# Kernel optimization log

Measured on AMD Instinct MI355X. Metric: run time of the kernel, lower is better.

Reference implementation:

```python
import jax, jax.numpy as jnp
import numpy as np

TEMPERATURE = 0.5
EPS = 1e-8  # torch CosineSimilarity eps


def setup_inputs() -> dict:
    key = jax.random.key(0)
    # x holds 2*batch_size concatenated embeddings (two augmented views)
    x = jax.random.normal(key, (4096, 512), dtype=jnp.float32)
    return {"x": x}


def reference(x) -> jnp.ndarray:
    n2 = x.shape[0]          # 2N rows
    n = n2 // 2
    # cosine similarity: normalize rows (clamped norm as in torch), then GEMM
    norms = jnp.maximum(jnp.linalg.norm(x, axis=1, keepdims=True), EPS)
    xn = x / norms
    sim = jnp.einsum('id,jd->ij', xn, xn) / TEMPERATURE  # [2N, 2N]
    # positive logit for row i is sim[i, (i+N) mod 2N]
    idx = jnp.arange(n2)
    pos = sim[idx, (idx + n) % n2]
    # CE with label 0 over logits = [pos, negatives]; since the logit set for
    # row i is exactly {sim[i, j] : j != i}, CE_i = logsumexp_{j!=i} sim[i,j] - pos_i
    sim_masked = jnp.where(jnp.eye(n2, dtype=bool), -jnp.inf, sim)
    lse = jax.nn.logsumexp(sim_masked, axis=1)
    # criterion uses reduction='sum' then divides by bsz -> mean
    return jnp.mean(lse - pos)
```

## Files before the change

kernel.cpp:

```cpp
#include <hip/hip_runtime.h>
#include <hip/hip_bf16.h>
#include <math.h>

typedef __bf16 bf16_t;
typedef __bf16 bf16x8 __attribute__((ext_vector_type(8)));
typedef float f32x4 __attribute__((ext_vector_type(4)));

#define N2 4096
#define NHALF 2048
#define DIM 512
#define TEMP_INV 2.0f

__global__ __launch_bounds__(256) void k_prep(const float* __restrict__ x,
                                              bf16_t* __restrict__ xn,
                                              float* __restrict__ pos,
                                              float* __restrict__ diag,
                                              float* __restrict__ rowsum) {
    const int pair = blockIdx.x * 4 + (threadIdx.x >> 6);
    const int lane = threadIdx.x & 63;
    const int rowi = pair;
    const int rowp = pair + NHALF;

    const float4* xi = reinterpret_cast<const float4*>(x + (size_t)rowi * DIM);
    const float4* xp = reinterpret_cast<const float4*>(x + (size_t)rowp * DIM);
    float4 a0 = xi[lane * 2], a1 = xi[lane * 2 + 1];
    float4 b0 = xp[lane * 2], b1 = xp[lane * 2 + 1];

    float ssi = a0.x*a0.x + a0.y*a0.y + a0.z*a0.z + a0.w*a0.w
              + a1.x*a1.x + a1.y*a1.y + a1.z*a1.z + a1.w*a1.w;
    float ssp = b0.x*b0.x + b0.y*b0.y + b0.z*b0.z + b0.w*b0.w
              + b1.x*b1.x + b1.y*b1.y + b1.z*b1.z + b1.w*b1.w;
    float dot = a0.x*b0.x + a0.y*b0.y + a0.z*b0.z + a0.w*b0.w
              + a1.x*b1.x + a1.y*b1.y + a1.z*b1.z + a1.w*b1.w;
#pragma unroll
    for (int off = 32; off; off >>= 1) {
        ssi += __shfl_xor(ssi, off, 64);
        ssp += __shfl_xor(ssp, off, 64);
        dot += __shfl_xor(dot, off, 64);
    }
    const float ni = fmaxf(sqrtf(ssi), 1e-8f);
    const float np = fmaxf(sqrtf(ssp), 1e-8f);
    const float sci = 1.0f / ni, scp = 1.0f / np;

    float va[8] = {a0.x, a0.y, a0.z, a0.w, a1.x, a1.y, a1.z, a1.w};
    float vb[8] = {b0.x, b0.y, b0.z, b0.w, b1.x, b1.y, b1.z, b1.w};
    bf16x8 oi, op;
    float dii = 0.0f, dpp = 0.0f;
#pragma unroll
    for (int t = 0; t < 8; ++t) {
        oi[t] = (bf16_t)(va[t] * sci);
        op[t] = (bf16_t)(vb[t] * scp);
        float fi = (float)oi[t], fp_ = (float)op[t];
        dii += fi * fi;
        dpp += fp_ * fp_;
    }
    *reinterpret_cast<bf16x8*>(xn + (size_t)rowi * DIM + lane * 8) = oi;
    *reinterpret_cast<bf16x8*>(xn + (size_t)rowp * DIM + lane * 8) = op;
#pragma unroll
    for (int off = 32; off; off >>= 1) {
        dii += __shfl_xor(dii, off, 64);
        dpp += __shfl_xor(dpp, off, 64);
    }
    if (lane == 0) {
        const float pv = TEMP_INV * dot * sci * scp;
        pos[rowi] = pv;
        pos[rowp] = pv;
        diag[rowi] = TEMP_INV * dii;
        diag[rowp] = TEMP_INV * dpp;
    }
    if (threadIdx.x < 8) rowsum[blockIdx.x * 8 + threadIdx.x] = 0.0f;
}

__device__ __forceinline__ void load_lds16(const bf16_t* g, bf16_t* l) {
    __builtin_amdgcn_global_load_lds(
        (const __attribute__((address_space(1))) unsigned int*)g,
        (__attribute__((address_space(3))) unsigned int*)l,
        16, 0, 0);
}

__global__ __launch_bounds__(256) void k_simgemm(const bf16_t* __restrict__ xn,
                                                 float* __restrict__ rowsum) {
    __shared__ bf16_t As[2][128 * 64];
    __shared__ bf16_t Bs[2][128 * 64];
    __shared__ float  rpA[128];
    __shared__ float  rpB[128];

    const int t = blockIdx.x;
    int bn = (int)((sqrtf(8.0f * (float)t + 1.0f) - 1.0f) * 0.5f);
    while ((bn * (bn + 1)) / 2 > t) --bn;
    while (((bn + 1) * (bn + 2)) / 2 <= t) ++bn;
    const int bm = t - (bn * (bn + 1)) / 2;
    const bool diagb = (bm == bn);

    const int tid  = threadIdx.x;
    const int lane = tid & 63;
    const int wid  = tid >> 6;
    const int wr   = wid >> 1;
    const int wc   = wid & 1;
    const int q    = lane >> 4;
    const int l15  = lane & 15;

    if (tid < 128) { rpA[tid] = 0.0f; rpB[tid] = 0.0f; }

    const int sRow = tid >> 3;
    const int sCol = (tid & 7) * 8;
    const bf16_t* gA = xn + (size_t)(bm * 128 + sRow) * DIM + sCol;
    const bf16_t* gB = xn + (size_t)(bn * 128 + sRow) * DIM + sCol;

    f32x4 acc[4][4] = {};

#pragma unroll
    for (int c = 0; c < 4; ++c) {
        load_lds16(gA + (size_t)(c * 32) * DIM, &As[0][c * 2048 + tid * 8]);
        load_lds16(gB + (size_t)(c * 32) * DIM, &Bs[0][c * 2048 + tid * 8]);
    }
    __syncthreads();

    for (int kt = 0; kt < 8; ++kt) {
        const int cur = kt & 1;
        if (kt < 7) {
            const bf16_t* gA1 = gA + (size_t)(kt + 1) * 64;
            const bf16_t* gB1 = gB + (size_t)(kt + 1) * 64;
#pragma unroll
            for (int c = 0; c < 4; ++c) {
                load_lds16(gA1 + (size_t)(c * 32) * DIM,
                           &As[cur ^ 1][c * 2048 + tid * 8]);
                load_lds16(gB1 + (size_t)(c * 32) * DIM,
                           &Bs[cur ^ 1][c * 2048 + tid * 8]);
            }
        }
#pragma unroll
        for (int kk = 0; kk < 2; ++kk) {
            bf16x8 af[4], bv[4];
#pragma unroll
            for (int mt = 0; mt < 4; ++mt)
                af[mt] = *reinterpret_cast<const bf16x8*>(
                    &As[cur][(wr * 64 + mt * 16 + l15) * 64 + kk * 32 + q * 8]);
#pragma unroll
            for (int nt = 0; nt < 4; ++nt)
                bv[nt] = *reinterpret_cast<const bf16x8*>(
                    &Bs[cur][(wc * 64 + nt * 16 + l15) * 64 + kk * 32 + q * 8]);
#pragma unroll
            for (int mt = 0; mt < 4; ++mt)
#pragma unroll
                for (int nt = 0; nt < 4; ++nt)
                    acc[mt][nt] = __builtin_amdgcn_mfma_f32_16x16x32_bf16(
                        af[mt], bv[nt], acc[mt][nt], 0, 0, 0);
        }
        __syncthreads();
    }

    float colacc[4] = {0.0f, 0.0f, 0.0f, 0.0f};
#pragma unroll
    for (int mt = 0; mt < 4; ++mt) {
        float rowp[4] = {0.0f, 0.0f, 0.0f, 0.0f};
#pragma unroll
        for (int nt = 0; nt < 4; ++nt)
#pragma unroll
            for (int r = 0; r < 4; ++r) {
                float e = __expf(TEMP_INV * acc[mt][nt][r]);
                rowp[r] += e;
                colacc[nt] += e;
            }
#pragma unroll
        for (int r = 0; r < 4; ++r) {
            float p = rowp[r];
            p += __shfl_xor(p, 1, 64);
            p += __shfl_xor(p, 2, 64);
            p += __shfl_xor(p, 4, 64);
            p += __shfl_xor(p, 8, 64);
            if (l15 == 0) atomicAdd(&rpA[wr * 64 + mt * 16 + q * 4 + r], p);
        }
    }
    if (!diagb) {
#pragma unroll
        for (int nt = 0; nt < 4; ++nt) {
            float c = colacc[nt];
            c += __shfl_xor(c, 16, 64);
            c += __shfl_xor(c, 32, 64);
            if (q == 0) atomicAdd(&rpB[wc * 64 + nt * 16 + l15], c);
        }
    }
    __syncthreads();
    if (tid < 128) {
        atomicAdd(&rowsum[bm * 128 + tid], rpA[tid]);
    } else if (!diagb) {
        atomicAdd(&rowsum[bn * 128 + (tid - 128)], rpB[tid - 128]);
    }
}

__global__ __launch_bounds__(256) void k_finalize(const float* __restrict__ rowsum,
                                                  const float* __restrict__ pos,
                                                  const float* __restrict__ diag,
                                                  float* __restrict__ out) {
    __shared__ float red[256];
    const float4* rs4 = reinterpret_cast<const float4*>(rowsum);
    const float4* ps4 = reinterpret_cast<const float4*>(pos);
    const float4* dg4 = reinterpret_cast<const float4*>(diag);
    float s = 0.0f;
#pragma unroll
    for (int it = 0; it < 4; ++it) {
        const int i = it * 256 + threadIdx.x;
        float4 r = rs4[i];
        float4 p = ps4[i];
        float4 d = dg4[i];
        s += __logf(r.x - __expf(d.x)) - p.x;
        s += __logf(r.y - __expf(d.y)) - p.y;
        s += __logf(r.z - __expf(d.z)) - p.z;
        s += __logf(r.w - __expf(d.w)) - p.w;
    }
    red[threadIdx.x] = s;
    __syncthreads();
    for (int st = 128; st; st >>= 1) {
        if (threadIdx.x < st) red[threadIdx.x] += red[threadIdx.x + st];
        __syncthreads();
    }
    if (threadIdx.x == 0) out[0] = red[0] / (float)N2;
}

extern "C" void kernel_launch(void* const* d_in, const int* in_sizes, int n_in,
                              void* d_out, int out_size, void* d_ws, size_t ws_size,
                              hipStream_t stream) {
    (void)in_sizes; (void)n_in; (void)out_size; (void)ws_size;
    const float* x = (const float*)d_in[0];
    float* out = (float*)d_out;

    char* ws = (char*)d_ws;
    bf16_t* xn     = (bf16_t*)ws;
    float*  rowsum = (float*)(ws + (size_t)N2 * DIM * 2);
    float*  pos    = rowsum + N2;
    float*  diag   = pos + N2;

    k_prep<<<512, 256, 0, stream>>>(x, xn, pos, diag, rowsum);
    k_simgemm<<<528, 256, 0, stream>>>(xn, rowsum);
    k_finalize<<<1, 256, 0, stream>>>(rowsum, pos, diag, out);
}
```

Before: 87.89 us.

## Halve K tile and use explicit vmcnt waits for overlapped LDS prefetch

Shrinks the shared-memory K tile from 64 to 32 columns, doubling the number of K steps to 16 and halving LDS usage per block. It replaces the full __syncthreads after each step with an s_waitcnt vmcnt(4) that waits only for the current buffer's loads, plus raw s_barrier calls. This lets the next tile's global-to-LDS loads stay in flight during compute and may raise occupancy. The cost is twice as many barriers. Correctness now depends on the hand-coded waitcnt and barrier ordering, including whether the LDS-zeroing of rpA/rpB is still ordered before its later use.

```diff
diff --git a/kernel.cpp b/kernel.cpp
--- a/kernel.cpp
+++ b/kernel.cpp
@@ -80,8 +80,8 @@
 
 __global__ __launch_bounds__(256) void k_simgemm(const bf16_t* __restrict__ xn,
                                                  float* __restrict__ rowsum) {
-    __shared__ bf16_t As[2][128 * 64];
-    __shared__ bf16_t Bs[2][128 * 64];
+    __shared__ bf16_t As[2][128 * 32];
+    __shared__ bf16_t Bs[2][128 * 32];
     __shared__ float  rpA[128];
     __shared__ float  rpB[128];
 
@@ -102,52 +102,48 @@
 
     if (tid < 128) { rpA[tid] = 0.0f; rpB[tid] = 0.0f; }
 
-    const int sRow = tid >> 3;
-    const int sCol = (tid & 7) * 8;
-    const bf16_t* gA = xn + (size_t)(bm * 128 + sRow) * DIM + sCol;
-    const bf16_t* gB = xn + (size_t)(bn * 128 + sRow) * DIM + sCol;
+    const bf16_t* gA = xn + (size_t)(bm * 128 + (tid >> 2)) * DIM + (tid & 3) * 8;
+    const bf16_t* gB = xn + (size_t)(bn * 128 + (tid >> 2)) * DIM + (tid & 3) * 8;
 
     f32x4 acc[4][4] = {};
 
-#pragma unroll
-    for (int c = 0; c < 4; ++c) {
-        load_lds16(gA + (size_t)(c * 32) * DIM, &As[0][c * 2048 + tid * 8]);
-        load_lds16(gB + (size_t)(c * 32) * DIM, &Bs[0][c * 2048 + tid * 8]);
-    }
-    __syncthreads();
-
-    for (int kt = 0; kt < 8; ++kt) {
+    load_lds16(gA,                    &As[0][tid * 8]);
+    load_lds16(gA + (size_t)64 * DIM, &As[0][2048 + tid * 8]);
+    load_lds16(gB,                    &Bs[0][tid * 8]);
+    load_lds16(gB + (size_t)64 * DIM, &Bs[0][2048 + tid * 8]);
+
+#pragma unroll
+    for (int kt = 0; kt < 16; ++kt) {
         const int cur = kt & 1;
-        if (kt < 7) {
-            const bf16_t* gA1 = gA + (size_t)(kt + 1) * 64;
-            const bf16_t* gB1 = gB + (size_t)(kt + 1) * 64;
-#pragma unroll
-            for (int c = 0; c < 4; ++c) {
-                load_lds16(gA1 + (size_t)(c * 32) * DIM,
-                           &As[cur ^ 1][c * 2048 + tid * 8]);
-                load_lds16(gB1 + (size_t)(c * 32) * DIM,
-                           &Bs[cur ^ 1][c * 2048 + tid * 8]);
-            }
+        if (kt < 15) {
+            const bf16_t* gA1 = gA + (size_t)(kt + 1) * 32;
+            const bf16_t* gB1 = gB + (size_t)(kt + 1) * 32;
+            load_lds16(gA1,                    &As[cur ^ 1][tid * 8]);
+            load_lds16(gA1 + (size_t)64 * DIM, &As[cur ^ 1][2048 + tid * 8]);
+            load_lds16(gB1,                    &Bs[cur ^ 1][tid * 8]);
+            load_lds16(gB1 + (size_t)64 * DIM, &Bs[cur ^ 1][2048 + tid * 8]);
+            asm volatile("s_waitcnt vmcnt(4)" ::: "memory");
+        } else {
+            asm volatile("s_waitcnt vmcnt(0)" ::: "memory");
         }
-#pragma unroll
-        for (int kk = 0; kk < 2; ++kk) {
-            bf16x8 af[4], bv[4];
-#pragma unroll
-            for (int mt = 0; mt < 4; ++mt)
-                af[mt] = *reinterpret_cast<const bf16x8*>(
-                    &As[cur][(wr * 64 + mt * 16 + l15) * 64 + kk * 32 + q * 8]);
+        __builtin_amdgcn_s_barrier();
+
+        bf16x8 af[4], bv[4];
+#pragma unroll
+        for (int mt = 0; mt < 4; ++mt)
+            af[mt] = *reinterpret_cast<const bf16x8*>(
+                &As[cur][(wr * 64 + mt * 16 + l15) * 32 + q * 8]);
+#pragma unroll
+        for (int nt = 0; nt < 4; ++nt)
+            bv[nt] = *reinterpret_cast<const bf16x8*>(
+                &Bs[cur][(wc * 64 + nt * 16 + l15) * 32 + q * 8]);
+#pragma unroll
+        for (int mt = 0; mt < 4; ++mt)
 #pragma unroll
             for (int nt = 0; nt < 4; ++nt)
-                bv[nt] = *reinterpret_cast<const bf16x8*>(
-                    &Bs[cur][(wc * 64 + nt * 16 + l15) * 64 + kk * 32 + q * 8]);
-#pragma unroll
-            for (int mt = 0; mt < 4; ++mt)
-#pragma unroll
-                for (int nt = 0; nt < 4; ++nt)
-                    acc[mt][nt] = __builtin_amdgcn_mfma_f32_16x16x32_bf16(
-                        af[mt], bv[nt], acc[mt][nt], 0, 0, 0);
-        }
-        __syncthreads();
+                acc[mt][nt] = __builtin_amdgcn_mfma_f32_16x16x32_bf16(
+                    af[mt], bv[nt], acc[mt][nt], 0, 0, 0);
+        __builtin_amdgcn_s_barrier();
     }
 
     float colacc[4] = {0.0f, 0.0f, 0.0f, 0.0f};
```

Result: faster. 84.25 us (-4.1%).
